# Optimization experiments

Hardware: AMD Instinct MI355X
Metric: run time of the kernel (lower is better)

The kernel has to match this reference:

```python
import jax, jax.numpy as jnp
import numpy as np

B, T, D, H, DK, DV, W, CHUNK = 2, 4096, 2048, 8, 128, 256, 4, 64
EPS_NORM = 1e-5
EPS_L2 = 1e-6


def silu(x):
    return x * jax.nn.sigmoid(x)


def causal_dwconv(x, w):
    # x: [B, T, C], w: [C, W]; torch Conv1d (cross-correlation) with left pad W-1,
    # keeping the first T outputs => strictly causal depthwise conv.
    Wk = w.shape[1]
    Tlen = x.shape[1]
    xp = jnp.pad(x, ((0, 0), (Wk - 1, 0), (0, 0)))
    return sum(xp[:, i:i + Tlen, :] * w[:, i] for i in range(Wk))


def l2norm(x):
    return x * jax.lax.rsqrt(jnp.sum(x * x, axis=-1, keepdims=True) + EPS_L2)


def delta_chunk(S, inp):
    # Gated delta-rule recurrence over one chunk. S: [B,H,DK,DV]
    # S_t = exp(g_t) * S_{t-1}; err = v_t - k_t^T S_t; S_t += k_t (beta_t * err)^T; o_t = q_t^T S_t
    def step(S, t):
        q_t, k_t, v_t, g_t, b_t = t
        S = S * jnp.exp(g_t)[..., None, None]
        err = v_t - jnp.einsum('bhk,bhkv->bhv', k_t, S)
        S = S + k_t[..., :, None] * (b_t[..., None] * err)[..., None, :]
        o_t = jnp.einsum('bhk,bhkv->bhv', q_t, S)
        return S, o_t
    return jax.lax.scan(step, S, inp)


def reference(x, Wq, Wk, Wv, Wb, Wa, Wg, Wo, conv_q, conv_k, conv_v, A_log, dt_bias, g_norm_w):
    # short causal depthwise conv + silu on q/k/v projections
    q = silu(causal_dwconv(x @ Wq, conv_q))
    k = silu(causal_dwconv(x @ Wk, conv_k))
    v = silu(causal_dwconv(x @ Wv, conv_v))
    beta = jax.nn.sigmoid(x @ Wb)                              # [B,T,H]
    g = -jnp.exp(A_log) * jax.nn.softplus(x @ Wa + dt_bias)   # [B,T,H], log-decay <= 0
    q = l2norm(q.reshape(B, T, H, DK)) * (DK ** -0.5)
    k = l2norm(k.reshape(B, T, H, DK))
    v = v.reshape(B, T, H, DV)

    def to_chunks(a):  # [B,T,...] -> [T//CHUNK, CHUNK, B, ...]
        return a.swapaxes(0, 1).reshape(T // CHUNK, CHUNK, a.shape[0], *a.shape[2:])

    inp = (to_chunks(q), to_chunks(k), to_chunks(v), to_chunks(g), to_chunks(beta))
    S0 = jnp.zeros((B, H, DK, DV), x.dtype)
    _, o = jax.lax.scan(jax.checkpoint(delta_chunk), S0, inp)  # o: [Nc,CHUNK,B,H,DV]
    o = o.reshape(T, B, H, DV).swapaxes(0, 1)                  # [B,T,H,DV]

    # per-head gated RMSNorm (FusedRMSNormGated with silu gate) then output projection
    gate = (x @ Wg).reshape(B, T, H, DV)
    o = o * jax.lax.rsqrt(jnp.mean(o * o, axis=-1, keepdims=True) + EPS_NORM)
    o = o * g_norm_w * silu(gate)
    return o.reshape(B, T, H * DV) @ Wo


def setup_inputs() -> dict:
    key = jax.random.key(0)
    ks = jax.random.split(key, 14)
    s = 0.02
    f = jnp.float32
    x = jax.random.normal(ks[0], (B, T, D), f)
    Wq = jax.random.normal(ks[1], (D, H * DK), f) * s
    Wk = jax.random.normal(ks[2], (D, H * DK), f) * s
    Wv = jax.random.normal(ks[3], (D, H * DV), f) * s
    Wb = jax.random.normal(ks[4], (D, H), f) * s
    Wa = jax.random.normal(ks[5], (D, H), f) * s
    Wg = jax.random.normal(ks[6], (D, H * DV), f) * s
    Wo = jax.random.normal(ks[7], (H * DV, D), f) * s
    conv_q = jax.random.normal(ks[8], (H * DK, W), f) * 0.2
    conv_k = jax.random.normal(ks[9], (H * DK, W), f) * 0.2
    conv_v = jax.random.normal(ks[10], (H * DV, W), f) * 0.2
    A_log = jnp.log(jax.random.uniform(ks[11], (H,), f, 1.0, 16.0))
    dt_bias = jax.random.normal(ks[12], (H,), f) * 0.5
    g_norm_w = jnp.ones((DV,), f)
    return dict(x=x, Wq=Wq, Wk=Wk, Wv=Wv, Wb=Wb, Wa=Wa, Wg=Wg, Wo=Wo,
                conv_q=conv_q, conv_k=conv_k, conv_v=conv_v,
                A_log=A_log, dt_bias=dt_bias, g_norm_w=g_norm_w)
```

## Files before the change

### kernel.cpp

```cpp
#include <hip/hip_runtime.h>
#include <cstdint>
#include <cstddef>

#define B_ 2
#define T_ 4096
#define D_ 2048
#define H_ 8
#define DK_ 128
#define DV_ 256
#define BT_ (B_*T_)
#define NQK_ 1024
#define NV_ 2048
#define N1_ 6144

typedef __bf16 bf16x8 __attribute__((ext_vector_type(8)));
typedef float f32x4 __attribute__((ext_vector_type(4)));

#define GAS __attribute__((address_space(1)))
#define LAS __attribute__((address_space(3)))

__device__ __forceinline__ float bfu(unsigned short u) {
  union { unsigned int i; float f; } c; c.i = ((unsigned int)u) << 16; return c.f;
}
__device__ __forceinline__ float bflo(unsigned int u) {
  union { unsigned int i; float f; } c; c.i = u << 16; return c.f;
}
__device__ __forceinline__ float bfhi(unsigned int u) {
  union { unsigned int i; float f; } c; c.i = u & 0xFFFF0000u; return c.f;
}
__device__ __forceinline__ unsigned short f2bf(float f) {
  union { float f; unsigned int i; } c; c.f = f;
  unsigned int x = c.i;
  x += 0x7FFFu + ((x >> 16) & 1u);
  return (unsigned short)(x >> 16);
}
__device__ __forceinline__ unsigned int pack2(float a, float b) {
  return (unsigned int)f2bf(a) | ((unsigned int)f2bf(b) << 16);
}
__device__ __forceinline__ float siluf(float x) { return x / (1.f + __expf(-x)); }
__device__ __forceinline__ float redsum32(float v) {
  #pragma unroll
  for (int m = 16; m >= 1; m >>= 1) v += __shfl_xor(v, m);
  return v;
}
__device__ __forceinline__ void async_copy16(void* lds, const void* gsrc) {
  __builtin_amdgcn_global_load_lds((const GAS unsigned int*)gsrc,
                                   (LAS unsigned int*)lds, 16, 0, 0);
}

template<int CTRL>
__device__ __forceinline__ float dpp_add(float x) {
  union { int i; float f; } a, r;
  a.f = x;
  r.i = __builtin_amdgcn_update_dpp(0, a.i, CTRL, 0xF, 0xF, true);
  return x + r.f;
}
__device__ __forceinline__ float red32_dpp(float x) {
  x = dpp_add<0x111>(x);
  x = dpp_add<0x112>(x);
  x = dpp_add<0x114>(x);
  x = dpp_add<0x118>(x);
  x = dpp_add<0x142>(x);
  return x;
}
__device__ __forceinline__ float bcast_halves(float x, int lane) {
  union { int i; float f; } a, lo, hi;
  a.f = x;
  lo.i = __builtin_amdgcn_readlane(a.i, 31);
  hi.i = __builtin_amdgcn_readlane(a.i, 63);
  return (lane & 32) ? hi.f : lo.f;
}

__global__ __launch_bounds__(256) void cast_x_kernel(const float* __restrict__ in,
                                                     unsigned short* __restrict__ out) {
  size_t i = ((size_t)blockIdx.x * 256 + threadIdx.x) * 4;
  float4 v = *(const float4*)(in + i);
  uint2 r;
  r.x = pack2(v.x, v.y);
  r.y = pack2(v.z, v.w);
  *(uint2*)(out + i) = r;
}

__global__ __launch_bounds__(256) void transpose_cast(const float* __restrict__ in,
                                                      unsigned short* __restrict__ out,
                                                      int R, int Cc) {
  __shared__ float tile[32][33];
  int c0 = blockIdx.x * 32, r0 = blockIdx.y * 32;
  int tx = threadIdx.x, ty = threadIdx.y;
  #pragma unroll
  for (int i = 0; i < 4; ++i)
    tile[ty + i*8][tx] = in[(size_t)(r0 + ty + i*8) * Cc + c0 + tx];
  __syncthreads();
  #pragma unroll
  for (int i = 0; i < 4; ++i)
    out[(size_t)(c0 + ty + i*8) * R + r0 + tx] = f2bf(tile[tx][ty + i*8]);
}

template<int BF16OUT>
__global__ __launch_bounds__(256) void gemm_kernel(
    const unsigned short* __restrict__ A,
    const unsigned short* __restrict__ Bt,
    void* __restrict__ Cout,
    int M, int N, int K)
{
  __shared__ __align__(16) unsigned short As[128][32];
  __shared__ __align__(16) unsigned short Bs[128][32];
  const int tid  = threadIdx.x;
  const int lane = tid & 63;
  const int wave = tid >> 6;
  const int wr = wave >> 1, wc = wave & 1;
  const int row0 = blockIdx.y * 128, col0 = blockIdx.x * 128;
  f32x4 acc[4][4];
  #pragma unroll
  for (int m = 0; m < 4; ++m)
    #pragma unroll
    for (int n = 0; n < 4; ++n)
      acc[m][n] = (f32x4){0.f, 0.f, 0.f, 0.f};

  const int fr = lane & 15;
  const int fq = lane >> 4;

  for (int k0 = 0; k0 < K; k0 += 32) {
    #pragma unroll
    for (int i = 0; i < 2; ++i) {
      int c = tid + i * 256;
      int r = c >> 2, o = (c & 3) * 8;
      async_copy16(&As[r][o], A  + (size_t)(row0 + r) * K + k0 + o);
      async_copy16(&Bs[r][o], Bt + (size_t)(col0 + r) * K + k0 + o);
    }
    asm volatile("s_waitcnt vmcnt(0)" ::: "memory");
    __syncthreads();
    bf16x8 af[4], bfr[4];
    #pragma unroll
    for (int m = 0; m < 4; ++m)
      af[m] = *(const bf16x8*)&As[wr*64 + m*16 + fr][fq*8];
    #pragma unroll
    for (int n = 0; n < 4; ++n)
      bfr[n] = *(const bf16x8*)&Bs[wc*64 + n*16 + fr][fq*8];
    #pragma unroll
    for (int m = 0; m < 4; ++m)
      #pragma unroll
      for (int n = 0; n < 4; ++n)
        acc[m][n] = __builtin_amdgcn_mfma_f32_16x16x32_bf16(af[m], bfr[n], acc[m][n], 0, 0, 0);
    __syncthreads();
  }
  const int fc = lane & 15, fg = lane >> 4;
  #pragma unroll
  for (int m = 0; m < 4; ++m)
    #pragma unroll
    for (int n = 0; n < 4; ++n)
      #pragma unroll
      for (int r = 0; r < 4; ++r) {
        size_t idx = (size_t)(row0 + wr*64 + m*16 + fg*4 + r) * N
                   + (col0 + wc*64 + n*16 + fc);
        if (BF16OUT) ((unsigned short*)Cout)[idx] = f2bf(acc[m][n][r]);
        else         ((float*)Cout)[idx]          = acc[m][n][r];
      }
}

__global__ __launch_bounds__(256) void beta_g_kernel(
    const float* __restrict__ x, const float* __restrict__ Wb, const float* __restrict__ Wa,
    const float* __restrict__ A_log, const float* __restrict__ dtb,
    float* __restrict__ beta, float* __restrict__ gmo)
{
  const int t = blockIdx.x;
  const int wave = threadIdx.x >> 6;
  const int lane = threadIdx.x & 63;
  const float* xr = x + (size_t)t * D_;
  float acc[4] = {0.f, 0.f, 0.f, 0.f};
  for (int k = lane; k < D_; k += 64) {
    float xv = xr[k];
    #pragma unroll
    for (int i = 0; i < 4; ++i) {
      int o = wave + 4 * i;
      float w = (o < 8) ? Wb[(size_t)k * 8 + o] : Wa[(size_t)k * 8 + (o - 8)];
      acc[i] += xv * w;
    }
  }
  #pragma unroll
  for (int i = 0; i < 4; ++i) {
    #pragma unroll
    for (int m = 32; m >= 1; m >>= 1) acc[i] += __shfl_xor(acc[i], m);
  }
  if (lane == 0) {
    #pragma unroll
    for (int i = 0; i < 4; ++i) {
      int o = wave + 4 * i;
      if (o < 8) {
        beta[(size_t)t * H_ + o] = 1.f / (1.f + __expf(-acc[i]));
      } else {
        int h = o - 8;
        float z = acc[i] + dtb[h];
        float sp = (z > 20.f) ? z : log1pf(__expf(z));
        gmo[(size_t)t * H_ + h] = __expf(-__expf(A_log[h]) * sp);
      }
    }
  }
}

__global__ __launch_bounds__(256) void conv_kernel(
    const unsigned short* __restrict__ Y1,
    const float* __restrict__ cq, const float* __restrict__ ck, const float* __restrict__ cv,
    float* __restrict__ qf, float* __restrict__ kf, float* __restrict__ vf)
{
  const int t  = blockIdx.x;
  const int tt = t & (T_ - 1);
  const int tid = threadIdx.x;
  const int c4 = tid * 4;
  const int c8 = tid * 8;

  float wqa[4][4], wka[4][4], wva[8][4];
  #pragma unroll
  for (int m = 0; m < 4; ++m) {
    float4 a = *(const float4*)(cq + (size_t)(c4 + m) * 4);
    wqa[m][0] = a.x; wqa[m][1] = a.y; wqa[m][2] = a.z; wqa[m][3] = a.w;
    float4 b = *(const float4*)(ck + (size_t)(c4 + m) * 4);
    wka[m][0] = b.x; wka[m][1] = b.y; wka[m][2] = b.z; wka[m][3] = b.w;
  }
  #pragma unroll
  for (int m = 0; m < 8; ++m) {
    float4 a = *(const float4*)(cv + (size_t)(c8 + m) * 4);
    wva[m][0] = a.x; wva[m][1] = a.y; wva[m][2] = a.z; wva[m][3] = a.w;
  }

  float aq[4] = {0,0,0,0}, ak[4] = {0,0,0,0}, av[8] = {0,0,0,0,0,0,0,0};
  #pragma unroll
  for (int i = 0; i < 4; ++i) {
    if (tt + i >= 3) {
      const unsigned short* row = Y1 + (size_t)(t + i - 3) * N1_;
      ushort4 yq = *(const ushort4*)(row + c4);
      ushort4 yk = *(const ushort4*)(row + NQK_ + c4);
      int4    yv = *(const int4*)(row + 2 * NQK_ + c8);
      float qv[4] = { bfu(yq.x), bfu(yq.y), bfu(yq.z), bfu(yq.w) };
      float kv[4] = { bfu(yk.x), bfu(yk.y), bfu(yk.z), bfu(yk.w) };
      unsigned int vu[4] = { (unsigned)yv.x, (unsigned)yv.y, (unsigned)yv.z, (unsigned)yv.w };
      float vv[8] = { bflo(vu[0]), bfhi(vu[0]), bflo(vu[1]), bfhi(vu[1]),
                      bflo(vu[2]), bfhi(vu[2]), bflo(vu[3]), bfhi(vu[3]) };
      #pragma unroll
      for (int m = 0; m < 4; ++m) { aq[m] += qv[m] * wqa[m][i]; ak[m] += kv[m] * wka[m][i]; }
      #pragma unroll
      for (int m = 0; m < 8; ++m) av[m] += vv[m] * wva[m][i];
    }
  }
  float sq[4], sk[4], ssq = 0.f, ssk = 0.f;
  #pragma unroll
  for (int m = 0; m < 4; ++m) {
    sq[m] = siluf(aq[m]); ssq += sq[m] * sq[m];
    sk[m] = siluf(ak[m]); ssk += sk[m] * sk[m];
  }
  ssq = redsum32(ssq);
  ssk = redsum32(ssk);
  float scq = rsqrtf(ssq + 1e-6f) * 0.08838834764831845f;
  float sck = rsqrtf(ssk + 1e-6f);
  float4 oq = { sq[0]*scq, sq[1]*scq, sq[2]*scq, sq[3]*scq };
  float4 ok = { sk[0]*sck, sk[1]*sck, sk[2]*sck, sk[3]*sck };
  *(float4*)(qf + (size_t)t * NQK_ + c4) = oq;
  *(float4*)(kf + (size_t)t * NQK_ + c4) = ok;
  float4 ov0 = { siluf(av[0]), siluf(av[1]), siluf(av[2]), siluf(av[3]) };
  float4 ov1 = { siluf(av[4]), siluf(av[5]), siluf(av[6]), siluf(av[7]) };
  *(float4*)(vf + (size_t)t * NV_ + c8)     = ov0;
  *(float4*)(vf + (size_t)t * NV_ + c8 + 4) = ov1;
}

__global__ __launch_bounds__(64) void delta_kernel(
    const float* __restrict__ qf, const float* __restrict__ kf,
    const float* __restrict__ vf,
    const float* __restrict__ gm, const float* __restrict__ beta,
    float* __restrict__ o)
{
  const int blk = blockIdx.x;
  const int bh = blk & 15;
  const int jp = blk >> 4;
  const int b = bh >> 3, h = bh & 7;
  const int lane = threadIdx.x;
  const int r = lane & 31;
  const int j = jp * 2 + (lane >> 5);

  const int SQK = H_ * DK_;
  const int SV  = H_ * DV_;

  const float* qp = qf + (size_t)(b * T_) * SQK + h * DK_ + r * 4;
  const float* kp = kf + (size_t)(b * T_) * SQK + h * DK_ + r * 4;
  const float* vp = vf + (size_t)(b * T_) * SV + h * DV_ + j;
  const float* gp = gm   + (size_t)(b * T_) * H_ + h;
  const float* bp = beta + (size_t)(b * T_) * H_ + h;
  float*       op = o  + (size_t)(b * T_) * SV + h * DV_ + j;

  float S0 = 0.f, S1 = 0.f, S2 = 0.f, S3 = 0.f;

  float4 kd0 = *(const float4*)kp,         qd0 = *(const float4*)qp;
  float  vv0 = *vp, bt0 = *bp, gm0 = *gp;
  float4 kd1 = *(const float4*)(kp + SQK), qd1 = *(const float4*)(qp + SQK);
  float  vv1 = vp[SV], bt1 = bp[H_], gm1 = gp[H_];
  float4 kd2, qd2, kd3, qd3;
  float  vv2, bt2, gm2, vv3, bt3, gm3;

  qp += 2 * SQK; kp += 2 * SQK; vp += 2 * SV; gp += 2 * H_; bp += 2 * H_;

#define PREF(SL, ROW) do { \
    kd##SL = *(const float4*)(kp + (ROW) * SQK); \
    qd##SL = *(const float4*)(qp + (ROW) * SQK); \
    vv##SL = vp[(ROW) * SV]; \
    bt##SL = bp[(ROW) * H_]; \
    gm##SL = gp[(ROW) * H_]; \
  } while (0)

#define STEP(SL) do { \
    float part = kd##SL.x*S0 + kd##SL.y*S1 + kd##SL.z*S2 + kd##SL.w*S3; \
    float dred = red32_dpp(part); \
    float dot0 = bcast_halves(dred, lane); \
    float u = bt##SL * (vv##SL - gm##SL * dot0); \
    S0 = gm##SL * S0 + kd##SL.x * u; \
    S1 = gm##SL * S1 + kd##SL.y * u; \
    S2 = gm##SL * S2 + kd##SL.z * u; \
    S3 = gm##SL * S3 + kd##SL.w * u; \
    float po = qd##SL.x*S0 + qd##SL.y*S1 + qd##SL.z*S2 + qd##SL.w*S3; \
    float od = red32_dpp(po); \
    if (r == 31) *op = od; \
    op += SV; \
  } while (0)

  for (int t = 0; t < T_; t += 4) {
    PREF(2, 0); STEP(0);
    PREF(3, 1); STEP(1);
    PREF(0, 2); STEP(2);
    PREF(1, 3); STEP(3);
    qp += 4 * SQK; kp += 4 * SQK; vp += 4 * SV; gp += 4 * H_; bp += 4 * H_;
  }
#undef PREF
#undef STEP
}

__global__ __launch_bounds__(256) void post_kernel(
    const float* __restrict__ o, const unsigned short* __restrict__ Y1,
    const float* __restrict__ gw, unsigned short* __restrict__ og)
{
  const int t = blockIdx.x;
  const int tid = threadIdx.x;
  const int e = tid * 8;
  float4 v0 = *(const float4*)(o + (size_t)t * NV_ + e);
  float4 v1 = *(const float4*)(o + (size_t)t * NV_ + e + 4);
  float v[8] = { v0.x, v0.y, v0.z, v0.w, v1.x, v1.y, v1.z, v1.w };
  float ss = 0.f;
  #pragma unroll
  for (int m = 0; m < 8; ++m) ss += v[m] * v[m];
  ss = redsum32(ss);
  float rms = rsqrtf(ss * (1.f / 256.f) + 1e-5f);
  int4 graw = *(const int4*)(Y1 + (size_t)t * N1_ + 4096 + e);
  unsigned int gu[4] = { (unsigned)graw.x, (unsigned)graw.y, (unsigned)graw.z, (unsigned)graw.w };
  float gv[8] = { bflo(gu[0]), bfhi(gu[0]), bflo(gu[1]), bfhi(gu[1]),
                  bflo(gu[2]), bfhi(gu[2]), bflo(gu[3]), bfhi(gu[3]) };
  const int dv = e & 255;
  float res[8];
  #pragma unroll
  for (int m = 0; m < 8; ++m) res[m] = v[m] * rms * gw[dv + m] * siluf(gv[m]);
  int4 outv;
  outv.x = (int)pack2(res[0], res[1]);
  outv.y = (int)pack2(res[2], res[3]);
  outv.z = (int)pack2(res[4], res[5]);
  outv.w = (int)pack2(res[6], res[7]);
  *(int4*)(og + (size_t)t * NV_ + e) = outv;
}

extern "C" void kernel_launch(void* const* d_in, const int* in_sizes, int n_in,
                              void* d_out, int out_size, void* d_ws, size_t ws_size,
                              hipStream_t stream)
{
  (void)in_sizes; (void)n_in; (void)out_size;
  const float* x     = (const float*)d_in[0];
  const float* Wq    = (const float*)d_in[1];
  const float* Wk    = (const float*)d_in[2];
  const float* Wv    = (const float*)d_in[3];
  const float* Wb    = (const float*)d_in[4];
  const float* Wa    = (const float*)d_in[5];
  const float* Wg    = (const float*)d_in[6];
  const float* Wo    = (const float*)d_in[7];
  const float* cq    = (const float*)d_in[8];
  const float* ck    = (const float*)d_in[9];
  const float* cv    = (const float*)d_in[10];
  const float* A_log = (const float*)d_in[11];
  const float* dtb   = (const float*)d_in[12];
  const float* gw    = (const float*)d_in[13];

  char* ws = (char*)d_ws;
  const size_t SZ_XB  = (size_t)BT_ * D_ * 2;
  const size_t SZ_WCT = (size_t)N1_ * D_ * 2;
  const size_t SZ_QF  = (size_t)BT_ * NQK_ * 4;
  const size_t SZ_KF  = (size_t)BT_ * NQK_ * 4;
  const size_t SZ_VF  = (size_t)BT_ * NV_ * 4;
  const size_t SZ_R1a = SZ_XB + SZ_WCT;
  const size_t SZ_R1b = SZ_QF + SZ_KF + SZ_VF;
  const size_t SZ_R1  = (SZ_R1a > SZ_R1b) ? SZ_R1a : SZ_R1b;
  const size_t SZ_WOT = (size_t)D_ * D_ * 2;
  const size_t SZ_BG  = (size_t)BT_ * H_ * 4;
  const size_t SZ_Y1  = (size_t)BT_ * N1_ * 2;

  const size_t OFF_WOT  = SZ_R1;
  const size_t OFF_BETA = OFF_WOT + SZ_WOT;
  const size_t OFF_GL   = OFF_BETA + SZ_BG;
  const size_t OFF_Y1   = OFF_GL + SZ_BG;
  const size_t WS_NEEDED = OFF_Y1 + SZ_Y1;
  if (ws_size < WS_NEEDED) return;

  unsigned short* xb  = (unsigned short*)(ws);
  unsigned short* Wct = (unsigned short*)(ws + SZ_XB);
  float* qf = (float*)(ws);
  float* kf = (float*)(ws + SZ_QF);
  float* vf = (float*)(ws + SZ_QF + SZ_KF);
  float* ov = vf;
  unsigned short* og  = (unsigned short*)(ws);
  unsigned short* Wot = (unsigned short*)(ws + OFF_WOT);
  float* beta = (float*)(ws + OFF_BETA);
  float* gl   = (float*)(ws + OFF_GL);
  unsigned short* Y1  = (unsigned short*)(ws + OFF_Y1);

  cast_x_kernel<<<(BT_ * D_) / 1024, 256, 0, stream>>>(x, xb);
  dim3 tb(32, 8);
  transpose_cast<<<dim3(1024/32, 2048/32), tb, 0, stream>>>(Wq, Wct, 2048, 1024);
  transpose_cast<<<dim3(1024/32, 2048/32), tb, 0, stream>>>(Wk, Wct + (size_t)1024 * 2048, 2048, 1024);
  transpose_cast<<<dim3(2048/32, 2048/32), tb, 0, stream>>>(Wv, Wct + (size_t)2048 * 2048, 2048, 2048);
  transpose_cast<<<dim3(2048/32, 2048/32), tb, 0, stream>>>(Wg, Wct + (size_t)4096 * 2048, 2048, 2048);
  transpose_cast<<<dim3(2048/32, 2048/32), tb, 0, stream>>>(Wo, Wot, 2048, 2048);

  gemm_kernel<1><<<dim3(N1_/128, BT_/128), 256, 0, stream>>>(xb, Wct, Y1, BT_, N1_, D_);
  beta_g_kernel<<<BT_, 256, 0, stream>>>(x, Wb, Wa, A_log, dtb, beta, gl);
  conv_kernel<<<BT_, 256, 0, stream>>>(Y1, cq, ck, cv, qf, kf, vf);
  delta_kernel<<<B_ * H_ * (DV_/2), 64, 0, stream>>>(qf, kf, vf, gl, beta, ov);
  post_kernel<<<BT_, 256, 0, stream>>>(ov, Y1, gw, og);
  gemm_kernel<0><<<dim3(D_/128, BT_/128), 256, 0, stream>>>(og, Wot, d_out, BT_, D_, D_);
}
```

Before: 2.011 ms.

## Rework delta recurrence to 16 lanes per column with 8-deep prefetch

The delta kernel now gives each state column 16 lanes holding 8 state rows each, instead of 32 lanes holding 4, so each wave covers four columns. The reduction becomes a 4-step row_ror DPP sum that leaves the result in every lane, which removes the readlane broadcast. Beta and the decay are interleaved into one float2 buffer, and the prefetch window grows from 2 to 8 timesteps. The intent is to shorten the serial per-step latency chain and to launch half as many blocks, at the cost of more registers per lane and less block-level parallelism.

```diff
diff --git a/kernel.cpp b/kernel.cpp
--- a/kernel.cpp
+++ b/kernel.cpp
@@ -55,20 +55,12 @@
   r.i = __builtin_amdgcn_update_dpp(0, a.i, CTRL, 0xF, 0xF, true);
   return x + r.f;
 }
-__device__ __forceinline__ float red32_dpp(float x) {
-  x = dpp_add<0x111>(x);
-  x = dpp_add<0x112>(x);
-  x = dpp_add<0x114>(x);
-  x = dpp_add<0x118>(x);
-  x = dpp_add<0x142>(x);
+__device__ __forceinline__ float red16_ror(float x) {
+  x = dpp_add<0x121>(x);
+  x = dpp_add<0x122>(x);
+  x = dpp_add<0x124>(x);
+  x = dpp_add<0x128>(x);
   return x;
-}
-__device__ __forceinline__ float bcast_halves(float x, int lane) {
-  union { int i; float f; } a, lo, hi;
-  a.f = x;
-  lo.i = __builtin_amdgcn_readlane(a.i, 31);
-  hi.i = __builtin_amdgcn_readlane(a.i, 63);
-  return (lane & 32) ? hi.f : lo.f;
 }
 
 __global__ __launch_bounds__(256) void cast_x_kernel(const float* __restrict__ in,
@@ -161,7 +153,7 @@
 __global__ __launch_bounds__(256) void beta_g_kernel(
     const float* __restrict__ x, const float* __restrict__ Wb, const float* __restrict__ Wa,
     const float* __restrict__ A_log, const float* __restrict__ dtb,
-    float* __restrict__ beta, float* __restrict__ gmo)
+    float* __restrict__ bg)
 {
   const int t = blockIdx.x;
   const int wave = threadIdx.x >> 6;
@@ -187,12 +179,12 @@
     for (int i = 0; i < 4; ++i) {
       int o = wave + 4 * i;
       if (o < 8) {
-        beta[(size_t)t * H_ + o] = 1.f / (1.f + __expf(-acc[i]));
+        bg[((size_t)t * H_ + o) * 2] = 1.f / (1.f + __expf(-acc[i]));
       } else {
         int h = o - 8;
         float z = acc[i] + dtb[h];
         float sp = (z > 20.f) ? z : log1pf(__expf(z));
-        gmo[(size_t)t * H_ + h] = __expf(-__expf(A_log[h]) * sp);
+        bg[((size_t)t * H_ + h) * 2 + 1] = __expf(-__expf(A_log[h]) * sp);
       }
     }
   }
@@ -264,68 +256,79 @@
 
 __global__ __launch_bounds__(64) void delta_kernel(
     const float* __restrict__ qf, const float* __restrict__ kf,
-    const float* __restrict__ vf,
-    const float* __restrict__ gm, const float* __restrict__ beta,
+    const float* __restrict__ vf, const float* __restrict__ bg,
     float* __restrict__ o)
 {
   const int blk = blockIdx.x;
   const int bh = blk & 15;
-  const int jp = blk >> 4;
+  const int jq = blk >> 4;
   const int b = bh >> 3, h = bh & 7;
   const int lane = threadIdx.x;
-  const int r = lane & 31;
-  const int j = jp * 2 + (lane >> 5);
+  const int r = lane & 15;
+  const int j = jq * 4 + (lane >> 4);
 
   const int SQK = H_ * DK_;
   const int SV  = H_ * DV_;
 
-  const float* qp = qf + (size_t)(b * T_) * SQK + h * DK_ + r * 4;
-  const float* kp = kf + (size_t)(b * T_) * SQK + h * DK_ + r * 4;
+  const float* qp = qf + (size_t)(b * T_) * SQK + h * DK_ + r * 8;
+  const float* kp = kf + (size_t)(b * T_) * SQK + h * DK_ + r * 8;
   const float* vp = vf + (size_t)(b * T_) * SV + h * DV_ + j;
-  const float* gp = gm   + (size_t)(b * T_) * H_ + h;
-  const float* bp = beta + (size_t)(b * T_) * H_ + h;
+  const float* gp = bg + ((size_t)(b * T_) * H_ + h) * 2;
   float*       op = o  + (size_t)(b * T_) * SV + h * DV_ + j;
 
-  float S0 = 0.f, S1 = 0.f, S2 = 0.f, S3 = 0.f;
-
-  float4 kd0 = *(const float4*)kp,         qd0 = *(const float4*)qp;
-  float  vv0 = *vp, bt0 = *bp, gm0 = *gp;
-  float4 kd1 = *(const float4*)(kp + SQK), qd1 = *(const float4*)(qp + SQK);
-  float  vv1 = vp[SV], bt1 = bp[H_], gm1 = gp[H_];
-  float4 kd2, qd2, kd3, qd3;
-  float  vv2, bt2, gm2, vv3, bt3, gm3;
-
-  qp += 2 * SQK; kp += 2 * SQK; vp += 2 * SV; gp += 2 * H_; bp += 2 * H_;
+  float4 Sa = {0,0,0,0}, Sb = {0,0,0,0};
+
+  float4 ka0,kb0,qa0,qb0, ka1,kb1,qa1,qb1, ka2,kb2,qa2,qb2, ka3,kb3,qa3,qb3,
+         ka4,kb4,qa4,qb4, ka5,kb5,qa5,qb5, ka6,kb6,qa6,qb6, ka7,kb7,qa7,qb7;
+  float  vv0,vv1,vv2,vv3,vv4,vv5,vv6,vv7;
+  float2 bgv0,bgv1,bgv2,bgv3,bgv4,bgv5,bgv6,bgv7;
 
 #define PREF(SL, ROW) do { \
-    kd##SL = *(const float4*)(kp + (ROW) * SQK); \
-    qd##SL = *(const float4*)(qp + (ROW) * SQK); \
+    ka##SL = *(const float4*)(kp + (ROW) * SQK); \
+    kb##SL = *(const float4*)(kp + (ROW) * SQK + 4); \
+    qa##SL = *(const float4*)(qp + (ROW) * SQK); \
+    qb##SL = *(const float4*)(qp + (ROW) * SQK + 4); \
     vv##SL = vp[(ROW) * SV]; \
-    bt##SL = bp[(ROW) * H_]; \
-    gm##SL = gp[(ROW) * H_]; \
+    bgv##SL = *(const float2*)(gp + (ROW) * (H_ * 2)); \
   } while (0)
 
 #define STEP(SL) do { \
-    float part = kd##SL.x*S0 + kd##SL.y*S1 + kd##SL.z*S2 + kd##SL.w*S3; \
-    float dred = red32_dpp(part); \
-    float dot0 = bcast_halves(dred, lane); \
-    float u = bt##SL * (vv##SL - gm##SL * dot0); \
-    S0 = gm##SL * S0 + kd##SL.x * u; \
-    S1 = gm##SL * S1 + kd##SL.y * u; \
-    S2 = gm##SL * S2 + kd##SL.z * u; \
-    S3 = gm##SL * S3 + kd##SL.w * u; \
-    float po = qd##SL.x*S0 + qd##SL.y*S1 + qd##SL.z*S2 + qd##SL.w*S3; \
-    float od = red32_dpp(po); \
-    if (r == 31) *op = od; \
+    float p0 = ka##SL.x*Sa.x, p1 = ka##SL.y*Sa.y, p2 = ka##SL.z*Sa.z, p3 = ka##SL.w*Sa.w; \
+    float p4 = kb##SL.x*Sb.x, p5 = kb##SL.y*Sb.y, p6 = kb##SL.z*Sb.z, p7 = kb##SL.w*Sb.w; \
+    float part = ((p0 + p1) + (p2 + p3)) + ((p4 + p5) + (p6 + p7)); \
+    float dot = red16_ror(part); \
+    float gm = bgv##SL.y; \
+    float u = bgv##SL.x * fmaf(-gm, dot, vv##SL); \
+    Sa.x = fmaf(gm, Sa.x, ka##SL.x * u); \
+    Sa.y = fmaf(gm, Sa.y, ka##SL.y * u); \
+    Sa.z = fmaf(gm, Sa.z, ka##SL.z * u); \
+    Sa.w = fmaf(gm, Sa.w, ka##SL.w * u); \
+    Sb.x = fmaf(gm, Sb.x, kb##SL.x * u); \
+    Sb.y = fmaf(gm, Sb.y, kb##SL.y * u); \
+    Sb.z = fmaf(gm, Sb.z, kb##SL.z * u); \
+    Sb.w = fmaf(gm, Sb.w, kb##SL.w * u); \
+    float o0 = qa##SL.x*Sa.x, o1 = qa##SL.y*Sa.y, o2 = qa##SL.z*Sa.z, o3 = qa##SL.w*Sa.w; \
+    float o4 = qb##SL.x*Sb.x, o5 = qb##SL.y*Sb.y, o6 = qb##SL.z*Sb.z, o7 = qb##SL.w*Sb.w; \
+    float pov = ((o0 + o1) + (o2 + o3)) + ((o4 + o5) + (o6 + o7)); \
+    float od = red16_ror(pov); \
+    if (r == 0) *op = od; \
     op += SV; \
   } while (0)
 
-  for (int t = 0; t < T_; t += 4) {
-    PREF(2, 0); STEP(0);
-    PREF(3, 1); STEP(1);
-    PREF(0, 2); STEP(2);
-    PREF(1, 3); STEP(3);
-    qp += 4 * SQK; kp += 4 * SQK; vp += 4 * SV; gp += 4 * H_; bp += 4 * H_;
+  PREF(0,0); PREF(1,1); PREF(2,2); PREF(3,3);
+  PREF(4,4); PREF(5,5); PREF(6,6); PREF(7,7);
+  qp += 8 * SQK; kp += 8 * SQK; vp += 8 * SV; gp += 8 * (H_ * 2);
+
+  for (int t = 0; t < T_; t += 8) {
+    STEP(0); PREF(0,0);
+    STEP(1); PREF(1,1);
+    STEP(2); PREF(2,2);
+    STEP(3); PREF(3,3);
+    STEP(4); PREF(4,4);
+    STEP(5); PREF(5,5);
+    STEP(6); PREF(6,6);
+    STEP(7); PREF(7,7);
+    qp += 8 * SQK; kp += 8 * SQK; vp += 8 * SV; gp += 8 * (H_ * 2);
   }
 #undef PREF
 #undef STEP
@@ -392,13 +395,12 @@
   const size_t SZ_R1b = SZ_QF + SZ_KF + SZ_VF;
   const size_t SZ_R1  = (SZ_R1a > SZ_R1b) ? SZ_R1a : SZ_R1b;
   const size_t SZ_WOT = (size_t)D_ * D_ * 2;
-  const size_t SZ_BG  = (size_t)BT_ * H_ * 4;
+  const size_t SZ_BG  = (size_t)BT_ * H_ * 8;
   const size_t SZ_Y1  = (size_t)BT_ * N1_ * 2;
 
-  const size_t OFF_WOT  = SZ_R1;
-  const size_t OFF_BETA = OFF_WOT + SZ_WOT;
-  const size_t OFF_GL   = OFF_BETA + SZ_BG;
-  const size_t OFF_Y1   = OFF_GL + SZ_BG;
+  const size_t OFF_WOT = SZ_R1;
+  const size_t OFF_BG  = OFF_WOT + SZ_WOT;
+  const size_t OFF_Y1  = OFF_BG + SZ_BG;
   const size_t WS_NEEDED = OFF_Y1 + SZ_Y1;
   if (ws_size < WS_NEEDED) return;
 
@@ -410,8 +412,7 @@
   float* ov = vf;
   unsigned short* og  = (unsigned short*)(ws);
   unsigned short* Wot = (unsigned short*)(ws + OFF_WOT);
-  float* beta = (float*)(ws + OFF_BETA);
-  float* gl   = (float*)(ws + OFF_GL);
+  float* bg   = (float*)(ws + OFF_BG);
   unsigned short* Y1  = (unsigned short*)(ws + OFF_Y1);
 
   cast_x_kernel<<<(BT_ * D_) / 1024, 256, 0, stream>>>(x, xb);
@@ -423,9 +424,9 @@
   transpose_cast<<<dim3(2048/32, 2048/32), tb, 0, stream>>>(Wo, Wot, 2048, 2048);
 
   gemm_kernel<1><<<dim3(N1_/128, BT_/128), 256, 0, stream>>>(xb, Wct, Y1, BT_, N1_, D_);
-  beta_g_kernel<<<BT_, 256, 0, stream>>>(x, Wb, Wa, A_log, dtb, beta, gl);
+  beta_g_kernel<<<BT_, 256, 0, stream>>>(x, Wb, Wa, A_log, dtb, bg);
   conv_kernel<<<BT_, 256, 0, stream>>>(Y1, cq, ck, cv, qf, kf, vf);
-  delta_kernel<<<B_ * H_ * (DV_/2), 64, 0, stream>>>(qf, kf, vf, gl, beta, ov);
+  delta_kernel<<<B_ * H_ * (DV_/4), 64, 0, stream>>>(qf, kf, vf, bg, ov);
   post_kernel<<<BT_, 256, 0, stream>>>(ov, Y1, gw, og);
   gemm_kernel<0><<<dim3(D_/128, BT_/128), 256, 0, stream>>>(og, Wot, d_out, BT_, D_, D_);
 }
```

New measurement: 1.958 ms. 1.03x faster.
